# Optimization experiments

Measured on AMD Instinct MI355X. Metric: run time of the kernel, lower is better.

## Reference

```python
import jax, jax.numpy as jnp
import numpy as np

B, T = 64, 4096
K = 67            # 25 body + 21 + 21 hand keypoints
D = 256           # first_layer_size
C = 7             # num_classes
THR = 0.1         # confidence_threshold
EPS = 1e-5        # BatchNorm eps


def setup_inputs() -> dict:
    key = jax.random.key(0)
    ks = jax.random.split(key, 8)
    body = jax.random.normal(ks[0], (B, T, 75), dtype=jnp.float32)
    hand_right = jax.random.normal(ks[1], (B, T, 63), dtype=jnp.float32)
    hand_left = jax.random.normal(ks[2], (B, T, 63), dtype=jnp.float32)
    length = jax.random.randint(ks[3], (B,), 1, T + 1, dtype=jnp.int64)
    W1 = jax.random.normal(ks[4], (2 * K, D), dtype=jnp.float32) * 0.05
    b1 = jnp.zeros((D,), dtype=jnp.float32)
    gamma = jnp.ones((D,), dtype=jnp.float32)
    beta = jnp.zeros((D,), dtype=jnp.float32)
    Wc = jax.random.normal(ks[5], (D, C), dtype=jnp.float32) * 0.05
    bc = jnp.zeros((C,), dtype=jnp.float32)
    return {"body": body, "hand_right": hand_right, "hand_left": hand_left,
            "length": length, "W1": W1, "b1": b1, "gamma": gamma,
            "beta": beta, "Wc": Wc, "bc": bc}


def reference(body, hand_right, hand_left, length, W1, b1, gamma, beta, Wc, bc):
    # concat keypoint streams -> [B, T, 3K] -> [B, T, K, 3]
    feats = jnp.concatenate([body, hand_right, hand_left], axis=2)
    feats = feats.reshape(feats.shape[0], feats.shape[1], -1, 3)
    x, y, conf = feats[..., 0], feats[..., 1], feats[..., 2]
    conf = (conf > THR).astype(feats.dtype)
    # gate coords by confidence, flatten to [B, T, 2K]
    pos = jnp.stack([x * conf, y * conf], axis=3)
    pos = pos.reshape(pos.shape[0], pos.shape[1], -1)
    # static MLP: Linear + ReLU -> [B, T, D]
    sf = jax.nn.relu(jnp.einsum("btf,fd->btd", pos, W1) + b1)
    # masked max pool over valid timesteps (vectorized segment-max)
    mask = jnp.arange(sf.shape[1])[None, :] < length[:, None]      # [B, T]
    pooled = jnp.max(jnp.where(mask[:, :, None], sf, -jnp.inf), axis=1)  # [B, D]
    # BatchNorm1d (training mode: batch statistics)
    mean = pooled.mean(axis=0)
    var = pooled.var(axis=0)
    bn = (pooled - mean) / jnp.sqrt(var + EPS) * gamma + beta
    # classifier
    return bn @ Wc + bc
```

## Files before the change

kernel.cpp:

```cpp
#include <hip/hip_runtime.h>
#include <hip/hip_bf16.h>

#define B_   64
#define T_   4096
#define F_   134
#define FP_  160
#define D_   256
#define C_   7
#define THR_ 0.1f
#define EPS_ 1e-5f
#define NQ_  16

typedef __bf16 bf16x8 __attribute__((ext_vector_type(8)));
typedef float  f32x4  __attribute__((ext_vector_type(4)));

typedef __attribute__((address_space(1))) const unsigned int guint;
typedef __attribute__((address_space(3))) unsigned int luint;

#define FBAR() asm volatile("s_waitcnt vmcnt(0) lgkmcnt(0)\n\ts_barrier" ::: "memory")
#define LBAR() asm volatile("s_waitcnt lgkmcnt(0)\n\ts_barrier" ::: "memory")


__global__ void convert_w1(const float* __restrict__ W1, __bf16* __restrict__ W1bf) {
    __shared__ float tile[32][33];
    const int d0 = blockIdx.x * 32, f0 = blockIdx.y * 32;
    const int tx = threadIdx.x & 31, ty = threadIdx.x >> 5;
#pragma unroll
    for (int r = 0; r < 32; r += 8) {
        int f = f0 + ty + r;
        tile[ty + r][tx] = (f < F_) ? W1[f * D_ + d0 + tx] : 0.f;
    }
    __syncthreads();
#pragma unroll
    for (int r = 0; r < 32; r += 8) {
        int d = d0 + ty + r;
        W1bf[d * FP_ + f0 + tx] = (__bf16)tile[tx][ty + r];
    }
}

__global__ __launch_bounds__(256, 2)
void fused_mlp_pool(const float* __restrict__ body,
                    const float* __restrict__ hr,
                    const float* __restrict__ hl,
                    const int*   __restrict__ length,
                    const float* __restrict__ b1,
                    const __bf16* __restrict__ W1bf,
                    float* __restrict__ pooled)
{
    const int p = blockIdx.x;
    const int q = p >> 6;
    const int r = p & 63;

    const int tid  = threadIdx.x;
    const int wave = tid >> 6;
    const int lane = tid & 63;
    const int quad = lane >> 4;
    const int l16  = lane & 15;
    const int dbase = wave * 64;

    const int L1 = length[1];
    unsigned int mask = 0;
    unsigned long long len01 = 0, len23 = 0;
#pragma unroll
    for (int i = 0; i < 8; i++) {
        int bi = (r + i) & 63;
        int li = (L1 == 0) ? length[2 * bi] : length[bi];
        int ji = q + 16 * i;
        if (ji * 32 < li) mask |= (1u << i);
        if (i < 4) len01 |= (unsigned long long)(unsigned)li << (16 * i);
        else       len23 |= (unsigned long long)(unsigned)li << (16 * (i - 4));
    }
    const int m = __popc(mask);
    if (m == 0) return;

    __shared__ __align__(16) float  raw[2][6432];
    __shared__ __align__(16) __bf16 As2[2][5120];

    const long rowstride = (long)T_;

    auto stage = [&](int c, int bufi) {
        const int  bb = (r + c) & 63;
        const long t0 = (long)(q + 16 * c) * 32;
        const float* bodyt = body + (bb * rowstride + t0) * 75;
        const float* hrt   = hr   + (bb * rowstride + t0) * 63;
        const float* hlt   = hl   + (bb * rowstride + t0) * 63;
        char* rw = (char*)raw[bufi];
        for (int i = wave; i < 10; i += 4) {
            int off = i * 256 + lane * 4;
            if (off < 2400)
                __builtin_amdgcn_global_load_lds((guint*)(bodyt + off),
                                                 (luint*)(rw + off * 4), 16, 0, 0);
        }
        for (int i = wave; i < 8; i += 4) {
            int off = i * 256 + lane * 4;
            if (off < 2016) {
                __builtin_amdgcn_global_load_lds((guint*)(hrt + off),
                                                 (luint*)(rw + 9600 + off * 4), 16, 0, 0);
                __builtin_amdgcn_global_load_lds((guint*)(hlt + off),
                                                 (luint*)(rw + 17664 + off * 4), 16, 0, 0);
            }
        }
    };

    auto nth = [&](int n) -> int {
        unsigned int t = mask;
        for (int k = 0; k < n; k++) t &= t - 1;
        return __ffs(t) - 1;
    };

    int cs  = nth(0);
    int cs1 = (m > 1) ? nth(1) : -1;
    stage(cs, 0);
    if (m > 1) stage(cs1, 1);

    bf16x8 bfrag[4][5];
    float  b1v[4];
#pragma unroll
    for (int n = 0; n < 4; n++) {
        int d = dbase + n * 16 + l16;
        const __bf16* wp = W1bf + d * FP_ + quad * 8;
#pragma unroll
        for (int kt = 0; kt < 5; kt++)
            bfrag[n][kt] = *(const bf16x8*)(wp + kt * 32);
        b1v[n] = b1[d];
    }

    int roffv[8], wv[8];
    {
        const int t  = ((tid >> 5) & 3) * 8 + ((tid >> 2) & 7);
        const int kb = ((tid >> 7) & 1) * 4 + (tid & 3);
#pragma unroll
        for (int it = 0; it < 8; it++) {
            int k = it * 8 + kb;
            roffv[it] = (k < 25) ? t * 75 + 3 * k
                       : (k < 46) ? 2400 + t * 63 + 3 * (k - 25)
                                  : 4416 + t * 63 + 3 * (k - 46);
            wv[it] = ((t >> 4) * 5 + (k >> 4)) * 256
                   + (((k >> 2) & 3) * 16 + (t & 15)) * 4 + (k & 3);
        }
    }
    int roff_c = 0, w_c = 0;
    if (tid < 96) {
        int t = tid & 31, k = 64 + (tid >> 5);
        roff_c = 4416 + t * 63 + 3 * (k - 46);
        w_c = ((t >> 4) * 5 + (k >> 4)) * 256
            + (((k >> 2) & 3) * 16 + (t & 15)) * 4 + (k & 3);
    }

    for (int i = tid; i < 832; i += 256) {
        int bufi = (i >= 416);
        int ii = i - bufi * 416;
        int t = ii & 31, kp = 67 + (ii >> 5);
        int w = ((t >> 4) * 5 + (kp >> 4)) * 256
              + (((kp >> 2) & 3) * 16 + (t & 15)) * 4 + (kp & 3);
        ((unsigned int*)As2[bufi])[w] = 0u;
    }

    auto repack = [&](int bufi) {
        const float* rw = raw[bufi];
        __bf16* A = As2[bufi];
#pragma unroll
        for (int it = 0; it < 8; it++) {
            float x = rw[roffv[it]], y = rw[roffv[it] + 1], cf = rw[roffv[it] + 2];
            bool g = cf > THR_;
            unsigned short ux = __builtin_bit_cast(unsigned short, (__bf16)(g ? x : 0.f));
            unsigned short uy = __builtin_bit_cast(unsigned short, (__bf16)(g ? y : 0.f));
            ((unsigned int*)A)[wv[it]] = (unsigned int)ux | ((unsigned int)uy << 16);
        }
        if (tid < 96) {
            float x = rw[roff_c], y = rw[roff_c + 1], cf = rw[roff_c + 2];
            bool g = cf > THR_;
            unsigned short ux = __builtin_bit_cast(unsigned short, (__bf16)(g ? x : 0.f));
            unsigned short uy = __builtin_bit_cast(unsigned short, (__bf16)(g ? y : 0.f));
            ((unsigned int*)A)[w_c] = (unsigned int)ux | ((unsigned int)uy << 16);
        }
    };

    FBAR();
    repack(0);
    LBAR();

    for (int s = 0; s < m; s++) {
        const int  bufc = s & 1;
        const bool hn   = (s + 1 < m);
        const bool hn2  = (s + 2 < m);
        int cs2 = -1;
        if (hn2) {
            cs2 = cs1 + 1 + (__ffs(mask >> (cs1 + 1)) - 1);
            stage(cs2, bufc);
        }

        if (hn) repack(bufc ^ 1);

        __builtin_amdgcn_s_setprio(1);
        f32x4 acc[2][4];
#pragma unroll
        for (int mm = 0; mm < 2; mm++)
#pragma unroll
            for (int n = 0; n < 4; n++)
                acc[mm][n] = (f32x4){0.f, 0.f, 0.f, 0.f};
#pragma unroll
        for (int kt = 0; kt < 5; kt++) {
#pragma unroll
            for (int mm = 0; mm < 2; mm++) {
                bf16x8 a = *(const bf16x8*)(As2[bufc] + (mm * 5 + kt) * 512 + lane * 8);
#pragma unroll
                for (int n = 0; n < 4; n++)
                    acc[mm][n] = __builtin_amdgcn_mfma_f32_16x16x32_bf16(a, bfrag[n][kt], acc[mm][n], 0, 0, 0);
            }
        }
        __builtin_amdgcn_s_setprio(0);

        const int bb   = (r + cs) & 63;
        const int lenb = (int)((cs < 4 ? (len01 >> (cs * 16))
                                       : (len23 >> ((cs - 4) * 16))) & 0xFFFFull);
        const int tt0  = (q + 16 * cs) * 32;
        float rmax[4] = {0.f, 0.f, 0.f, 0.f};
#pragma unroll
        for (int mm = 0; mm < 2; mm++) {
            int trow0 = tt0 + mm * 16 + quad * 4;
#pragma unroll
            for (int rr = 0; rr < 4; rr++) {
                bool valid = (trow0 + rr) < lenb;
#pragma unroll
                for (int n = 0; n < 4; n++) {
                    float v = acc[mm][n][rr] + b1v[n];
                    v = (v > 0.f) ? v : 0.f;
                    rmax[n] = (valid && v > rmax[n]) ? v : rmax[n];
                }
            }
        }
#pragma unroll
        for (int n = 0; n < 4; n++) {
            rmax[n] = fmaxf(rmax[n], __shfl_xor(rmax[n], 16, 64));
            rmax[n] = fmaxf(rmax[n], __shfl_xor(rmax[n], 32, 64));
        }
        float rsel = (quad == 0) ? rmax[0] : (quad == 1) ? rmax[1]
                   : (quad == 2) ? rmax[2] : rmax[3];

        if (hn) FBAR();

        atomicMax((unsigned int*)(pooled + bb * D_ + tid),
                  __float_as_uint(rsel));

        cs = cs1; cs1 = cs2;
    }
}

__global__ void bn_classifier(const float* __restrict__ pooled,
                              const float* __restrict__ gamma,
                              const float* __restrict__ beta,
                              const float* __restrict__ Wc,
                              const float* __restrict__ bc,
                              float* __restrict__ out)
{
    __shared__ float scale_s[D_], shift_s[D_];
    const int tid = threadIdx.x;
    float s = 0.f, ss = 0.f;
#pragma unroll 8
    for (int b = 0; b < B_; b++) {
        float v = pooled[b * D_ + tid];
        s += v; ss += v * v;
    }
    float mean = s * (1.f / B_);
    float var  = ss * (1.f / B_) - mean * mean;
    var = fmaxf(var, 0.f);
    float sc = gamma[tid] * rsqrtf(var + EPS_);
    scale_s[tid] = sc;
    shift_s[tid] = beta[tid] - mean * sc;

    const int wv = tid >> 6, ln = tid & 63;
    float wcr[4][C_];
#pragma unroll
    for (int j = 0; j < 4; j++)
#pragma unroll
        for (int c = 0; c < C_; c++)
            wcr[j][c] = Wc[(ln * 4 + j) * C_ + c];
    __syncthreads();

    for (int b = wv * 16; b < wv * 16 + 16; b++) {
        float4 v = *(const float4*)(pooled + b * D_ + ln * 4);
        float q[4];
        q[0] = v.x * scale_s[ln * 4 + 0] + shift_s[ln * 4 + 0];
        q[1] = v.y * scale_s[ln * 4 + 1] + shift_s[ln * 4 + 1];
        q[2] = v.z * scale_s[ln * 4 + 2] + shift_s[ln * 4 + 2];
        q[3] = v.w * scale_s[ln * 4 + 3] + shift_s[ln * 4 + 3];
        float p[C_];
#pragma unroll
        for (int c = 0; c < C_; c++) p[c] = 0.f;
#pragma unroll
        for (int j = 0; j < 4; j++)
#pragma unroll
            for (int c = 0; c < C_; c++)
                p[c] += q[j] * wcr[j][c];
#pragma unroll
        for (int c = 0; c < C_; c++) {
#pragma unroll
            for (int off = 1; off < 64; off <<= 1)
                p[c] += __shfl_xor(p[c], off, 64);
        }
        if (ln == 0) {
#pragma unroll
            for (int c = 0; c < C_; c++)
                out[b * C_ + c] = p[c] + bc[c];
        }
    }
}

extern "C" void kernel_launch(void* const* d_in, const int* in_sizes, int n_in,
                              void* d_out, int out_size, void* d_ws, size_t ws_size,
                              hipStream_t stream) {
    const float* body   = (const float*)d_in[0];
    const float* hr     = (const float*)d_in[1];
    const float* hl     = (const float*)d_in[2];
    const int*   length = (const int*)  d_in[3];
    const float* W1     = (const float*)d_in[4];
    const float* b1     = (const float*)d_in[5];
    const float* gamma  = (const float*)d_in[6];
    const float* beta   = (const float*)d_in[7];
    const float* Wc     = (const float*)d_in[8];
    const float* bc     = (const float*)d_in[9];
    float* out = (float*)d_out;

    float*  pooled = (float*)d_ws;
    __bf16* W1bf   = (__bf16*)((char*)d_ws + 65536);

    hipMemsetAsync(d_ws, 0, 65536, stream);
    convert_w1<<<dim3(8, 5), dim3(256), 0, stream>>>(W1, W1bf);
    fused_mlp_pool<<<dim3(NQ_ * 64), dim3(256), 0, stream>>>(body, hr, hl, length, b1, W1bf, pooled);
    bn_classifier<<<dim3(1), dim3(256), 0, stream>>>(pooled, gamma, beta, Wc, bc, out);
}
```

Baseline: 233.0 us.

## Replace LDS staging with register-prefetched strided loads and raise occupancy

Drops the raw-float LDS staging buffers that were filled with global_load_lds, and has each thread load its own (x,y,conf) triples straight into registers one chunk ahead. The triples are gated and packed into the bf16 A tile after the MFMA and atomic of the current chunk. With the ~51KB raw buffers gone, LDS use falls enough that launch bounds go from 2 to 3 blocks per CU. The cost is uncoalesced 12-byte strided global loads in place of 16-byte contiguous bulk copies, plus extra registers holding the prefetched values.

Result: slower. 280.9 us (+20.5%).

```diff
diff --git a/kernel.cpp b/kernel.cpp
--- a/kernel.cpp
+++ b/kernel.cpp
@@ -14,10 +14,8 @@
 typedef __bf16 bf16x8 __attribute__((ext_vector_type(8)));
 typedef float  f32x4  __attribute__((ext_vector_type(4)));
 
-typedef __attribute__((address_space(1))) const unsigned int guint;
-typedef __attribute__((address_space(3))) unsigned int luint;
-
-#define FBAR() asm volatile("s_waitcnt vmcnt(0) lgkmcnt(0)\n\ts_barrier" ::: "memory")
+struct __attribute__((packed, aligned(4))) F3 { float x, y, c; };
+
 #define LBAR() asm volatile("s_waitcnt lgkmcnt(0)\n\ts_barrier" ::: "memory")
 
 
@@ -38,7 +36,7 @@
     }
 }
 
-__global__ __launch_bounds__(256, 2)
+__global__ __launch_bounds__(256, 3)
 void fused_mlp_pool(const float* __restrict__ body,
                     const float* __restrict__ hr,
                     const float* __restrict__ hl,
@@ -73,45 +71,62 @@
     const int m = __popc(mask);
     if (m == 0) return;
 
-    __shared__ __align__(16) float  raw[2][6432];
     __shared__ __align__(16) __bf16 As2[2][5120];
 
-    const long rowstride = (long)T_;
-
-    auto stage = [&](int c, int bufi) {
+    const int t  = ((tid >> 5) & 3) * 8 + ((tid >> 2) & 7);
+    const int kb = ((tid >> 7) & 1) * 4 + (tid & 3);
+    const float* gb[8];
+    bool  s75[8];
+    int   wv[8];
+#pragma unroll
+    for (int it = 0; it < 8; it++) {
+        int k = it * 8 + kb;
+        if (k < 25)      { gb[it] = body + 3 * k;        s75[it] = true;  }
+        else if (k < 46) { gb[it] = hr + 3 * (k - 25);   s75[it] = false; }
+        else             { gb[it] = hl + 3 * (k - 46);   s75[it] = false; }
+        wv[it] = ((t >> 4) * 5 + (k >> 4)) * 256
+               + (((k >> 2) & 3) * 16 + (t & 15)) * 4 + (k & 3);
+    }
+    const float* gb_c = nullptr; int w_c = 0, t_c = 0;
+    if (tid < 96) {
+        t_c = tid & 31; int k = 64 + (tid >> 5);
+        gb_c = hl + 3 * (k - 46);
+        w_c = ((t_c >> 4) * 5 + (k >> 4)) * 256
+            + (((k >> 2) & 3) * 16 + (t_c & 15)) * 4 + (k & 3);
+    }
+
+    F3 vbuf[8]; F3 vc3 = {0.f, 0.f, 0.f};
+    auto issue_loads = [&](int c) {
         const int  bb = (r + c) & 63;
-        const long t0 = (long)(q + 16 * c) * 32;
-        const float* bodyt = body + (bb * rowstride + t0) * 75;
-        const float* hrt   = hr   + (bb * rowstride + t0) * 63;
-        const float* hlt   = hl   + (bb * rowstride + t0) * 63;
-        char* rw = (char*)raw[bufi];
-        for (int i = wave; i < 10; i += 4) {
-            int off = i * 256 + lane * 4;
-            if (off < 2400)
-                __builtin_amdgcn_global_load_lds((guint*)(bodyt + off),
-                                                 (luint*)(rw + off * 4), 16, 0, 0);
-        }
-        for (int i = wave; i < 8; i += 4) {
-            int off = i * 256 + lane * 4;
-            if (off < 2016) {
-                __builtin_amdgcn_global_load_lds((guint*)(hrt + off),
-                                                 (luint*)(rw + 9600 + off * 4), 16, 0, 0);
-                __builtin_amdgcn_global_load_lds((guint*)(hlt + off),
-                                                 (luint*)(rw + 17664 + off * 4), 16, 0, 0);
-            }
-        }
+        const int  t0 = (q + 16 * c) * 32;
+        const long row = (long)bb * T_ + t0;
+        const long o75 = (row + t) * 75;
+        const long o63 = (row + t) * 63;
+#pragma unroll
+        for (int it = 0; it < 8; it++)
+            vbuf[it] = *(const F3*)(gb[it] + (s75[it] ? o75 : o63));
+        if (tid < 96) vc3 = *(const F3*)(gb_c + (row + t_c) * 63);
     };
 
-    auto nth = [&](int n) -> int {
-        unsigned int t = mask;
-        for (int k = 0; k < n; k++) t &= t - 1;
-        return __ffs(t) - 1;
+    auto pack = [&](int bufi) {
+        __bf16* A = As2[bufi];
+#pragma unroll
+        for (int it = 0; it < 8; it++) {
+            bool g = vbuf[it].c > THR_;
+            unsigned short ux = __builtin_bit_cast(unsigned short, (__bf16)(g ? vbuf[it].x : 0.f));
+            unsigned short uy = __builtin_bit_cast(unsigned short, (__bf16)(g ? vbuf[it].y : 0.f));
+            ((unsigned int*)A)[wv[it]] = (unsigned int)ux | ((unsigned int)uy << 16);
+        }
+        if (tid < 96) {
+            bool g = vc3.c > THR_;
+            unsigned short ux = __builtin_bit_cast(unsigned short, (__bf16)(g ? vc3.x : 0.f));
+            unsigned short uy = __builtin_bit_cast(unsigned short, (__bf16)(g ? vc3.y : 0.f));
+            ((unsigned int*)A)[w_c] = (unsigned int)ux | ((unsigned int)uy << 16);
+        }
     };
 
-    int cs  = nth(0);
-    int cs1 = (m > 1) ? nth(1) : -1;
-    stage(cs, 0);
-    if (m > 1) stage(cs1, 1);
+    int cs = __ffs(mask) - 1;
+    issue_loads(cs);
 
     bf16x8 bfrag[4][5];
     float  b1v[4];
@@ -125,72 +140,27 @@
         b1v[n] = b1[d];
     }
 
-    int roffv[8], wv[8];
-    {
-        const int t  = ((tid >> 5) & 3) * 8 + ((tid >> 2) & 7);
-        const int kb = ((tid >> 7) & 1) * 4 + (tid & 3);
-#pragma unroll
-        for (int it = 0; it < 8; it++) {
-            int k = it * 8 + kb;
-            roffv[it] = (k < 25) ? t * 75 + 3 * k
-                       : (k < 46) ? 2400 + t * 63 + 3 * (k - 25)
-                                  : 4416 + t * 63 + 3 * (k - 46);
-            wv[it] = ((t >> 4) * 5 + (k >> 4)) * 256
-                   + (((k >> 2) & 3) * 16 + (t & 15)) * 4 + (k & 3);
-        }
-    }
-    int roff_c = 0, w_c = 0;
-    if (tid < 96) {
-        int t = tid & 31, k = 64 + (tid >> 5);
-        roff_c = 4416 + t * 63 + 3 * (k - 46);
-        w_c = ((t >> 4) * 5 + (k >> 4)) * 256
-            + (((k >> 2) & 3) * 16 + (t & 15)) * 4 + (k & 3);
-    }
-
     for (int i = tid; i < 832; i += 256) {
         int bufi = (i >= 416);
         int ii = i - bufi * 416;
-        int t = ii & 31, kp = 67 + (ii >> 5);
-        int w = ((t >> 4) * 5 + (kp >> 4)) * 256
-              + (((kp >> 2) & 3) * 16 + (t & 15)) * 4 + (kp & 3);
+        int tt = ii & 31, kp = 67 + (ii >> 5);
+        int w = ((tt >> 4) * 5 + (kp >> 4)) * 256
+              + (((kp >> 2) & 3) * 16 + (tt & 15)) * 4 + (kp & 3);
         ((unsigned int*)As2[bufi])[w] = 0u;
     }
 
-    auto repack = [&](int bufi) {
-        const float* rw = raw[bufi];
-        __bf16* A = As2[bufi];
-#pragma unroll
-        for (int it = 0; it < 8; it++) {
-            float x = rw[roffv[it]], y = rw[roffv[it] + 1], cf = rw[roffv[it] + 2];
-            bool g = cf > THR_;
-            unsigned short ux = __builtin_bit_cast(unsigned short, (__bf16)(g ? x : 0.f));
-            unsigned short uy = __builtin_bit_cast(unsigned short, (__bf16)(g ? y : 0.f));
-            ((unsigned int*)A)[wv[it]] = (unsigned int)ux | ((unsigned int)uy << 16);
-        }
-        if (tid < 96) {
-            float x = rw[roff_c], y = rw[roff_c + 1], cf = rw[roff_c + 2];
-            bool g = cf > THR_;
-            unsigned short ux = __builtin_bit_cast(unsigned short, (__bf16)(g ? x : 0.f));
-            unsigned short uy = __builtin_bit_cast(unsigned short, (__bf16)(g ? y : 0.f));
-            ((unsigned int*)A)[w_c] = (unsigned int)ux | ((unsigned int)uy << 16);
-        }
-    };
-
-    FBAR();
-    repack(0);
+    pack(0);
     LBAR();
 
     for (int s = 0; s < m; s++) {
         const int  bufc = s & 1;
         const bool hn   = (s + 1 < m);
-        const bool hn2  = (s + 2 < m);
-        int cs2 = -1;
-        if (hn2) {
-            cs2 = cs1 + 1 + (__ffs(mask >> (cs1 + 1)) - 1);
-            stage(cs2, bufc);
-        }
-
-        if (hn) repack(bufc ^ 1);
+        int cs1 = -1;
+        if (hn) {
+            cs1 = cs + 1 + (__ffs(mask >> (cs + 1)) - 1);
+            issue_loads(cs1);
+            __builtin_amdgcn_sched_barrier(0);
+        }
 
         __builtin_amdgcn_s_setprio(1);
         f32x4 acc[2][4];
@@ -237,13 +207,14 @@
         }
         float rsel = (quad == 0) ? rmax[0] : (quad == 1) ? rmax[1]
                    : (quad == 2) ? rmax[2] : rmax[3];
-
-        if (hn) FBAR();
-
         atomicMax((unsigned int*)(pooled + bb * D_ + tid),
                   __float_as_uint(rsel));
 
-        cs = cs1; cs1 = cs2;
+        if (hn) {
+            pack(bufc ^ 1);
+            LBAR();
+            cs = cs1;
+        }
     }
 }
 
```
